# Optimization experiments

Measured on AMD Instinct MI355X. Metric: run time of the kernel, lower is better.

Reference implementation:

```python
import jax, jax.numpy as jnp
import numpy as np

WINDOW_SIZE = 11
SIGMA = 1.5
C1 = (0.01 * 1.0) ** 2
C2 = (0.03 * 1.0) ** 2


def _gauss1d(k, sigma):
    x = np.arange(k, dtype=np.float64) - k // 2
    g = np.exp(-(x ** 2) / (2.0 * sigma ** 2)) / (np.sqrt(2.0 * np.pi) * sigma)
    return (g / g.sum()).astype(np.float32)


def _blur3d(x, g):
    # Separable 3D Gaussian blur, SAME padding. Math-equal to the full 11^3
    # kernel conv in the torch code since the 3D window is an outer product
    # of the normalized 1D Gaussian (symmetric, so conv == cross-corr).
    k = g.shape[0]
    p = k // 2
    dn = ('NCDHW', 'OIDHW', 'NCDHW')
    for axis in range(3):
        shape = [1, 1, 1, 1, 1]
        shape[2 + axis] = k
        w = jnp.asarray(g).reshape(shape)
        pad = [(0, 0), (0, 0), (0, 0)]
        pad[axis] = (p, p)
        x = jax.lax.conv_general_dilated(x, w, (1, 1, 1), pad, dimension_numbers=dn)
    return x


def setup_inputs() -> dict:
    key = jax.random.key(0)
    k1, k2 = jax.random.split(key)
    shape = (4, 1, 192, 192, 192)
    gt = jax.random.uniform(k1, shape, dtype=jnp.float32)
    pred = jax.random.uniform(k2, shape, dtype=jnp.float32)
    return {"gt": gt, "pred": pred}


def reference(gt, pred):
    g = _gauss1d(WINDOW_SIZE, SIGMA)
    mux = _blur3d(gt, g)
    muy = _blur3d(pred, g)
    mux_sq = mux * mux
    muy_sq = muy * muy
    mux_muy = mux * muy
    sigmax_sq = _blur3d(gt * gt, g) - mux_sq
    sigmay_sq = _blur3d(pred * pred, g) - muy_sq
    sigmaxy = _blur3d(gt * pred, g) - mux_muy
    ssim_map = ((2.0 * mux_muy + C1) * (2.0 * sigmaxy + C2)) / (
        (mux_sq + muy_sq + C1) * (sigmax_sq + sigmay_sq + C2))
    return jnp.mean(1.0 - ssim_map)
```

## Files before the change

### kernel.cpp

```cpp
#include <hip/hip_runtime.h>
#include <hip/hip_fp16.h>
#include <math.h>

namespace {
constexpr int S = 192;
constexpr long long S2 = (long long)S * S;
constexpr long long S3 = (long long)S * S2;
constexpr int NB = 4;
constexpr int K = 11;
constexpr int R = 5;
constexpr int HCH = 48;
constexpr int DCH = 48;
constexpr float C1f = 1e-4f;
constexpr float C2f = 9e-4f;

struct GaussW { float g[K]; };

__global__ void k_init(double* acc) { *acc = 0.0; }

__global__ void k_final(const double* __restrict__ acc, float* __restrict__ out) {
  out[0] = (float)(acc[0] / (double)(NB * S3));
}


template <int N, bool GUARD>
__device__ __forceinline__ void loadA(const float* pg, const float* pp, int r0,
                                      int w, float (&la)[K], float (&lb)[K]) {
#pragma unroll
  for (int j = 0; j < N; ++j) {
    int r = r0 + j;
    bool ok = !GUARD || ((unsigned)r < (unsigned)S);
    la[j] = ok ? pg[(long long)r * S + w] : 0.f;
    lb[j] = ok ? pp[(long long)r * S + w] : 0.f;
  }
}

template <int N>
__device__ __forceinline__ void commitA(float2 (*rb)[208], int w,
                                        const float (&la)[K], const float (&lb)[K]) {
#pragma unroll
  for (int j = 0; j < N; ++j) rb[j][8 + w] = make_float2(la[j], lb[j]);
}

template <int NROWS, bool EMITALL>
__device__ __forceinline__ void consumeA(
    const float2 (*rb)[208], int w, const GaussW& Wt,
    float2 (&w01)[K], float2 (&w23)[K], float (&w4v)[K],
    __half2* p01, __half2* p23, __half* p4, long long obase, int hbase) {
#pragma unroll
  for (int j = 0; j < NROWS; ++j) {
    float2 s01 = make_float2(0.f, 0.f), s23 = make_float2(0.f, 0.f);
    float s4 = 0.f;
#pragma unroll
    for (int i = 0; i < K; ++i) {
      float2 ab = rb[j][w + 3 + i];
      float g = Wt.g[i];
      s01.x = fmaf(g, ab.x, s01.x);
      s01.y = fmaf(g, ab.y, s01.y);
      float ta = g * ab.x, tb = g * ab.y;
      s23.x = fmaf(ta, ab.x, s23.x);
      s23.y = fmaf(tb, ab.y, s23.y);
      s4 = fmaf(ta, ab.y, s4);
    }
    w01[j] = s01; w23[j] = s23; w4v[j] = s4;
    if (EMITALL || j == K - 1) {
      float2 m01 = make_float2(0.f, 0.f), m23 = make_float2(0.f, 0.f);
      float m4 = 0.f;
#pragma unroll
      for (int i = 0; i < K; ++i) {
        const int sl = (j + 1 + i) % K;
        float g = Wt.g[i];
        m01.x = fmaf(g, w01[sl].x, m01.x);
        m01.y = fmaf(g, w01[sl].y, m01.y);
        m23.x = fmaf(g, w23[sl].x, m23.x);
        m23.y = fmaf(g, w23[sl].y, m23.y);
        m4 = fmaf(g, w4v[sl], m4);
      }
      long long o = obase + (long long)(hbase + j) * S;
      p01[o] = __floats2half2_rn(m01.x, m01.y);
      p23[o] = __floats2half2_rn(m23.x, m23.y);
      p4[o] = __float2half(m4);
    }
  }
}

__global__ __launch_bounds__(192) void k_blurWH(
    const float* __restrict__ gt, const float* __restrict__ pr,
    __half2* __restrict__ p01, __half2* __restrict__ p23, __half* __restrict__ p4,
    long long in_base, GaussW Wt) {
  __shared__ float2 rowbuf[2][K][208];
  const int w = threadIdx.x;
  const int dz = blockIdx.x;
  const int h0 = (int)blockIdx.y * HCH;
  const long long n = blockIdx.z;
  const float* pg = gt + in_base + (n * S + dz) * S2;
  const float* pp = pr + in_base + (n * S + dz) * S2;
  const long long obase = (n * S + dz) * S2 + w;

  if (w < 176) {
    int j = w >> 4, q = w & 15;
    int idx = (q < 8) ? q : (192 + q);
    rowbuf[0][j][idx] = make_float2(0.f, 0.f);
    rowbuf[1][j][idx] = make_float2(0.f, 0.f);
  }

  float2 w01[K], w23[K];
  float w4v[K];
  float la[K], lb[K];

  loadA<K, true>(pg, pp, h0 - R, w, la, lb);
  commitA<K>(rowbuf[0], w, la, lb);
  __syncthreads();
  loadA<K, false>(pg, pp, h0 + 6, w, la, lb);
  consumeA<K, false>(rowbuf[0], w, Wt, w01, w23, w4v, p01, p23, p4, obase, h0 - 10);
  commitA<K>(rowbuf[1], w, la, lb);
  __syncthreads();
  loadA<K, false>(pg, pp, h0 + 17, w, la, lb);
  consumeA<K, true>(rowbuf[1], w, Wt, w01, w23, w4v, p01, p23, p4, obase, h0 + 1);
  commitA<K>(rowbuf[0], w, la, lb);
  __syncthreads();
  loadA<K, false>(pg, pp, h0 + 28, w, la, lb);
  consumeA<K, true>(rowbuf[0], w, Wt, w01, w23, w4v, p01, p23, p4, obase, h0 + 12);
  commitA<K>(rowbuf[1], w, la, lb);
  __syncthreads();
  loadA<K, true>(pg, pp, h0 + 39, w, la, lb);
  consumeA<K, true>(rowbuf[1], w, Wt, w01, w23, w4v, p01, p23, p4, obase, h0 + 23);
  commitA<K>(rowbuf[0], w, la, lb);
  __syncthreads();
  loadA<3, true>(pg, pp, h0 + 50, w, la, lb);
  consumeA<K, true>(rowbuf[0], w, Wt, w01, w23, w4v, p01, p23, p4, obase, h0 + 34);
  commitA<3>(rowbuf[1], w, la, lb);
  __syncthreads();
  consumeA<3, true>(rowbuf[1], w, Wt, w01, w23, w4v, p01, p23, p4, obase, h0 + 45);
}


template <int N, bool GUARD>
__device__ __forceinline__ void stageB(const __half2* q01, const __half2* q23,
                                       const __half* q4, int plane0,
                                       __half2 (&sa)[K], __half2 (&sb)[K],
                                       __half (&se)[K]) {
  const __half2 z2 = __floats2half2_rn(0.f, 0.f);
  const __half z1 = __float2half(0.f);
#pragma unroll
  for (int j = 0; j < N; ++j) {
    int d = plane0 + j;
    bool ok = !GUARD || ((unsigned)d < (unsigned)S);
    long long o = (long long)d * S2;
    sa[j] = ok ? q01[o] : z2;
    sb[j] = ok ? q23[o] : z2;
    se[j] = ok ? q4[o] : z1;
  }
}

template <int NOUT>
__device__ __forceinline__ void consumeB(
    const __half2 (&sa)[K], const __half2 (&sb)[K], const __half (&se)[K],
    const GaussW& Wt, float2 (&r01)[K], float2 (&r23)[K], float (&r4)[K],
    double& lsum) {
  float fsum = 0.f;
#pragma unroll
  for (int j = 0; j < NOUT; ++j) {
    const int sw = (10 + j) % K;
    r01[sw] = __half22float2(sa[j]);
    r23[sw] = __half22float2(sb[j]);
    r4[sw] = __half2float(se[j]);
    float2 m01 = make_float2(0.f, 0.f), m23 = make_float2(0.f, 0.f);
    float m4 = 0.f;
#pragma unroll
    for (int i = 0; i < K; ++i) {
      const int sl = (j + i) % K;
      float g = Wt.g[i];
      m01.x = fmaf(g, r01[sl].x, m01.x);
      m01.y = fmaf(g, r01[sl].y, m01.y);
      m23.x = fmaf(g, r23[sl].x, m23.x);
      m23.y = fmaf(g, r23[sl].y, m23.y);
      m4 = fmaf(g, r4[sl], m4);
    }
    float mux = m01.x, muy = m01.y, bxx = m23.x, byy = m23.y, bxy = m4;
    float mux2 = mux * mux, muy2 = muy * muy, muxy = mux * muy;
    float sx = bxx - mux2, sy = byy - muy2, sxy = bxy - muxy;
    float num = fmaf(2.f, muxy, C1f) * fmaf(2.f, sxy, C2f);
    float den = (mux2 + muy2 + C1f) * (sx + sy + C2f);
    fsum += 1.f - num * __builtin_amdgcn_rcpf(den);
  }
  lsum += (double)fsum;
}

__global__ __launch_bounds__(192) void k_blurD_ssim(
    const __half2* __restrict__ p01, const __half2* __restrict__ p23,
    const __half* __restrict__ p4, double* __restrict__ acc, GaussW Wt) {
  const int w = threadIdx.x;
  const int h = blockIdx.x;
  const long long n = blockIdx.y;
  const int d0 = (int)blockIdx.z * DCH;
  const long long base = n * S3 + (long long)h * S + w;
  const __half2* q01 = p01 + base;
  const __half2* q23 = p23 + base;
  const __half* q4 = p4 + base;

  float2 r01[K], r23[K];
  float r4[K];
#pragma unroll
  for (int c = 0; c < K - 1; ++c) {
    int d = d0 - R + c;
    if ((unsigned)d < (unsigned)S) {
      long long o = (long long)d * S2;
      r01[c] = __half22float2(q01[o]);
      r23[c] = __half22float2(q23[o]);
      r4[c] = __half2float(q4[o]);
    } else {
      r01[c] = make_float2(0.f, 0.f);
      r23[c] = make_float2(0.f, 0.f);
      r4[c] = 0.f;
    }
  }
  r01[K - 1] = make_float2(0.f, 0.f);
  r23[K - 1] = make_float2(0.f, 0.f);
  r4[K - 1] = 0.f;

  __half2 sa0[K], sb0[K], sa1[K], sb1[K];
  __half se0[K], se1[K];
  double lsum = 0.0;

  stageB<K, false>(q01, q23, q4, d0 + 5, sa0, sb0, se0);
  stageB<K, false>(q01, q23, q4, d0 + 16, sa1, sb1, se1);
  consumeB<K>(sa0, sb0, se0, Wt, r01, r23, r4, lsum);
  stageB<K, false>(q01, q23, q4, d0 + 27, sa0, sb0, se0);
  consumeB<K>(sa1, sb1, se1, Wt, r01, r23, r4, lsum);
  stageB<K, true>(q01, q23, q4, d0 + 38, sa1, sb1, se1);
  consumeB<K>(sa0, sb0, se0, Wt, r01, r23, r4, lsum);
  stageB<4, true>(q01, q23, q4, d0 + 49, sa0, sb0, se0);
  consumeB<K>(sa1, sb1, se1, Wt, r01, r23, r4, lsum);
  consumeB<4>(sa0, sb0, se0, Wt, r01, r23, r4, lsum);

  double v = lsum;
#pragma unroll
  for (int o = 32; o > 0; o >>= 1) v += __shfl_down(v, o, 64);
  __shared__ double wsum[3];
  int lane = threadIdx.x & 63, wv = threadIdx.x >> 6;
  if (lane == 0) wsum[wv] = v;
  __syncthreads();
  if (threadIdx.x == 0) atomicAdd(acc, wsum[0] + wsum[1] + wsum[2]);
}

}

extern "C" void kernel_launch(void* const* d_in, const int* in_sizes, int n_in,
                              void* d_out, int out_size, void* d_ws, size_t ws_size,
                              hipStream_t stream) {
  (void)in_sizes; (void)n_in; (void)out_size;
  const float* gt = (const float*)d_in[0];
  const float* pr = (const float*)d_in[1];
  float* out = (float*)d_out;
  double* acc = (double*)d_ws;

  GaussW W;
  {
    double gg[K], sum = 0.0;
    for (int i = 0; i < K; ++i) {
      double x = (double)(i - K / 2);
      gg[i] = exp(-(x * x) / (2.0 * 1.5 * 1.5)) / (sqrt(2.0 * M_PI) * 1.5);
      sum += gg[i];
    }
    for (int i = 0; i < K; ++i) W.g[i] = (float)(gg[i] / sum);
  }

  auto run = [&](long long base_n, int nb) {
    size_t vox = (size_t)nb * S3;
    __half2* p01 = (__half2*)((char*)d_ws + 256);
    __half2* p23 = p01 + vox;
    __half* p4 = (__half*)(p23 + vox);
    k_blurWH<<<dim3(S, S / HCH, nb), dim3(192), 0, stream>>>(
        gt, pr, p01, p23, p4, base_n * S3, W);
    k_blurD_ssim<<<dim3(S, nb, S / DCH), dim3(192), 0, stream>>>(
        p01, p23, p4, acc, W);
  };
  auto need = [](int nb) { return (size_t)256 + (size_t)nb * S3 * 10; };

  k_init<<<dim3(1), dim3(1), 0, stream>>>(acc);
  if (ws_size >= need(4)) {
    run(0, 4);
  } else if (ws_size >= need(2)) {
    run(0, 2);
    run(2, 2);
  } else {
    for (int g = 0; g < NB; ++g) run(g, 1);
  }
  k_final<<<dim3(1), dim3(1), 0, stream>>>(acc, out);
}
```

Baseline: 455.1 us.

## Interleave half2 intermediates into uint2, single-buffer rows, shrink H chunk

The two separate half2 intermediate planes (means and second moments) are merged into one interleaved uint2 array, so each voxel is written and read with a single 8-byte access instead of two 4-byte ones. The WH blur kernel drops its double-buffered row staging in favour of one shared buffer with load, sync, consume, sync phases, and the H chunk shrinks from 48 to 32 rows, giving more blocks. The intent is fewer memory transactions, lower LDS use and higher occupancy. In exchange, loads no longer overlap compute within a block, and the extra blocks recompute more halo rows.

```diff
diff --git a/kernel.cpp b/kernel.cpp
--- a/kernel.cpp
+++ b/kernel.cpp
@@ -9,7 +9,7 @@
 constexpr int NB = 4;
 constexpr int K = 11;
 constexpr int R = 5;
-constexpr int HCH = 48;
+constexpr int HCH = 32;
 constexpr int DCH = 48;
 constexpr float C1f = 1e-4f;
 constexpr float C2f = 9e-4f;
@@ -23,30 +23,26 @@
 }
 
 
-template <int N, bool GUARD>
-__device__ __forceinline__ void loadA(const float* pg, const float* pp, int r0,
-                                      int w, float (&la)[K], float (&lb)[K]) {
-#pragma unroll
-  for (int j = 0; j < N; ++j) {
+template <int NROWS, bool GUARD>
+__device__ __forceinline__ void stageA(const float* pg, const float* pp, int r0,
+                                       int w, float2 (*rb)[208]) {
+  float la[NROWS], lb[NROWS];
+#pragma unroll
+  for (int j = 0; j < NROWS; ++j) {
     int r = r0 + j;
     bool ok = !GUARD || ((unsigned)r < (unsigned)S);
     la[j] = ok ? pg[(long long)r * S + w] : 0.f;
     lb[j] = ok ? pp[(long long)r * S + w] : 0.f;
   }
-}
-
-template <int N>
-__device__ __forceinline__ void commitA(float2 (*rb)[208], int w,
-                                        const float (&la)[K], const float (&lb)[K]) {
-#pragma unroll
-  for (int j = 0; j < N; ++j) rb[j][8 + w] = make_float2(la[j], lb[j]);
+#pragma unroll
+  for (int j = 0; j < NROWS; ++j) rb[j][8 + w] = make_float2(la[j], lb[j]);
 }
 
 template <int NROWS, bool EMITALL>
 __device__ __forceinline__ void consumeA(
     const float2 (*rb)[208], int w, const GaussW& Wt,
     float2 (&w01)[K], float2 (&w23)[K], float (&w4v)[K],
-    __half2* p01, __half2* p23, __half* p4, long long obase, int hbase) {
+    uint2* p0123, __half* p4, long long obase, int hbase) {
 #pragma unroll
   for (int j = 0; j < NROWS; ++j) {
     float2 s01 = make_float2(0.f, 0.f), s23 = make_float2(0.f, 0.f);
@@ -77,8 +73,12 @@
         m4 = fmaf(g, w4v[sl], m4);
       }
       long long o = obase + (long long)(hbase + j) * S;
-      p01[o] = __floats2half2_rn(m01.x, m01.y);
-      p23[o] = __floats2half2_rn(m23.x, m23.y);
+      __half2 h01 = __floats2half2_rn(m01.x, m01.y);
+      __half2 h23 = __floats2half2_rn(m23.x, m23.y);
+      uint2 v;
+      v.x = __builtin_bit_cast(unsigned, h01);
+      v.y = __builtin_bit_cast(unsigned, h23);
+      p0123[o] = v;
       p4[o] = __float2half(m4);
     }
   }
@@ -86,9 +86,9 @@
 
 __global__ __launch_bounds__(192) void k_blurWH(
     const float* __restrict__ gt, const float* __restrict__ pr,
-    __half2* __restrict__ p01, __half2* __restrict__ p23, __half* __restrict__ p4,
+    uint2* __restrict__ p0123, __half* __restrict__ p4,
     long long in_base, GaussW Wt) {
-  __shared__ float2 rowbuf[2][K][208];
+  __shared__ float2 rowbuf[K][208];
   const int w = threadIdx.x;
   const int dz = blockIdx.x;
   const int h0 = (int)blockIdx.y * HCH;
@@ -99,71 +99,54 @@
 
   if (w < 176) {
     int j = w >> 4, q = w & 15;
-    int idx = (q < 8) ? q : (192 + q);
-    rowbuf[0][j][idx] = make_float2(0.f, 0.f);
-    rowbuf[1][j][idx] = make_float2(0.f, 0.f);
+    rowbuf[j][(q < 8) ? q : (192 + q)] = make_float2(0.f, 0.f);
   }
 
   float2 w01[K], w23[K];
   float w4v[K];
-  float la[K], lb[K];
-
-  loadA<K, true>(pg, pp, h0 - R, w, la, lb);
-  commitA<K>(rowbuf[0], w, la, lb);
-  __syncthreads();
-  loadA<K, false>(pg, pp, h0 + 6, w, la, lb);
-  consumeA<K, false>(rowbuf[0], w, Wt, w01, w23, w4v, p01, p23, p4, obase, h0 - 10);
-  commitA<K>(rowbuf[1], w, la, lb);
-  __syncthreads();
-  loadA<K, false>(pg, pp, h0 + 17, w, la, lb);
-  consumeA<K, true>(rowbuf[1], w, Wt, w01, w23, w4v, p01, p23, p4, obase, h0 + 1);
-  commitA<K>(rowbuf[0], w, la, lb);
-  __syncthreads();
-  loadA<K, false>(pg, pp, h0 + 28, w, la, lb);
-  consumeA<K, true>(rowbuf[0], w, Wt, w01, w23, w4v, p01, p23, p4, obase, h0 + 12);
-  commitA<K>(rowbuf[1], w, la, lb);
-  __syncthreads();
-  loadA<K, true>(pg, pp, h0 + 39, w, la, lb);
-  consumeA<K, true>(rowbuf[1], w, Wt, w01, w23, w4v, p01, p23, p4, obase, h0 + 23);
-  commitA<K>(rowbuf[0], w, la, lb);
-  __syncthreads();
-  loadA<3, true>(pg, pp, h0 + 50, w, la, lb);
-  consumeA<K, true>(rowbuf[0], w, Wt, w01, w23, w4v, p01, p23, p4, obase, h0 + 34);
-  commitA<3>(rowbuf[1], w, la, lb);
-  __syncthreads();
-  consumeA<3, true>(rowbuf[1], w, Wt, w01, w23, w4v, p01, p23, p4, obase, h0 + 45);
+
+  stageA<K, true>(pg, pp, h0 - R, w, rowbuf);
+  __syncthreads();
+  consumeA<K, false>(rowbuf, w, Wt, w01, w23, w4v, p0123, p4, obase, h0 - 10);
+  __syncthreads();
+  stageA<K, false>(pg, pp, h0 + 6, w, rowbuf);
+  __syncthreads();
+  consumeA<K, true>(rowbuf, w, Wt, w01, w23, w4v, p0123, p4, obase, h0 + 1);
+  __syncthreads();
+  stageA<K, false>(pg, pp, h0 + 17, w, rowbuf);
+  __syncthreads();
+  consumeA<K, true>(rowbuf, w, Wt, w01, w23, w4v, p0123, p4, obase, h0 + 12);
+  __syncthreads();
+  stageA<9, true>(pg, pp, h0 + 28, w, rowbuf);
+  __syncthreads();
+  consumeA<9, true>(rowbuf, w, Wt, w01, w23, w4v, p0123, p4, obase, h0 + 23);
 }
 
 
 template <int N, bool GUARD>
-__device__ __forceinline__ void stageB(const __half2* q01, const __half2* q23,
-                                       const __half* q4, int plane0,
-                                       __half2 (&sa)[K], __half2 (&sb)[K],
-                                       __half (&se)[K]) {
-  const __half2 z2 = __floats2half2_rn(0.f, 0.f);
-  const __half z1 = __float2half(0.f);
+__device__ __forceinline__ void stageB(const uint2* q0123, const __half* q4,
+                                       int plane0, uint2 (&sab)[K], __half (&se)[K]) {
 #pragma unroll
   for (int j = 0; j < N; ++j) {
     int d = plane0 + j;
     bool ok = !GUARD || ((unsigned)d < (unsigned)S);
     long long o = (long long)d * S2;
-    sa[j] = ok ? q01[o] : z2;
-    sb[j] = ok ? q23[o] : z2;
-    se[j] = ok ? q4[o] : z1;
+    sab[j] = ok ? q0123[o] : make_uint2(0u, 0u);
+    se[j] = ok ? q4[o] : __float2half(0.f);
   }
 }
 
 template <int NOUT>
 __device__ __forceinline__ void consumeB(
-    const __half2 (&sa)[K], const __half2 (&sb)[K], const __half (&se)[K],
+    const uint2 (&sab)[K], const __half (&se)[K],
     const GaussW& Wt, float2 (&r01)[K], float2 (&r23)[K], float (&r4)[K],
     double& lsum) {
   float fsum = 0.f;
 #pragma unroll
   for (int j = 0; j < NOUT; ++j) {
     const int sw = (10 + j) % K;
-    r01[sw] = __half22float2(sa[j]);
-    r23[sw] = __half22float2(sb[j]);
+    r01[sw] = __half22float2(__builtin_bit_cast(__half2, sab[j].x));
+    r23[sw] = __half22float2(__builtin_bit_cast(__half2, sab[j].y));
     r4[sw] = __half2float(se[j]);
     float2 m01 = make_float2(0.f, 0.f), m23 = make_float2(0.f, 0.f);
     float m4 = 0.f;
@@ -188,15 +171,14 @@
 }
 
 __global__ __launch_bounds__(192) void k_blurD_ssim(
-    const __half2* __restrict__ p01, const __half2* __restrict__ p23,
-    const __half* __restrict__ p4, double* __restrict__ acc, GaussW Wt) {
+    const uint2* __restrict__ p0123, const __half* __restrict__ p4,
+    double* __restrict__ acc, GaussW Wt) {
   const int w = threadIdx.x;
   const int h = blockIdx.x;
   const long long n = blockIdx.y;
   const int d0 = (int)blockIdx.z * DCH;
   const long long base = n * S3 + (long long)h * S + w;
-  const __half2* q01 = p01 + base;
-  const __half2* q23 = p23 + base;
+  const uint2* q0123 = p0123 + base;
   const __half* q4 = p4 + base;
 
   float2 r01[K], r23[K];
@@ -206,8 +188,9 @@
     int d = d0 - R + c;
     if ((unsigned)d < (unsigned)S) {
       long long o = (long long)d * S2;
-      r01[c] = __half22float2(q01[o]);
-      r23[c] = __half22float2(q23[o]);
+      uint2 v = q0123[o];
+      r01[c] = __half22float2(__builtin_bit_cast(__half2, v.x));
+      r23[c] = __half22float2(__builtin_bit_cast(__half2, v.y));
       r4[c] = __half2float(q4[o]);
     } else {
       r01[c] = make_float2(0.f, 0.f);
@@ -219,20 +202,20 @@
   r23[K - 1] = make_float2(0.f, 0.f);
   r4[K - 1] = 0.f;
 
-  __half2 sa0[K], sb0[K], sa1[K], sb1[K];
+  uint2 sab0[K], sab1[K];
   __half se0[K], se1[K];
   double lsum = 0.0;
 
-  stageB<K, false>(q01, q23, q4, d0 + 5, sa0, sb0, se0);
-  stageB<K, false>(q01, q23, q4, d0 + 16, sa1, sb1, se1);
-  consumeB<K>(sa0, sb0, se0, Wt, r01, r23, r4, lsum);
-  stageB<K, false>(q01, q23, q4, d0 + 27, sa0, sb0, se0);
-  consumeB<K>(sa1, sb1, se1, Wt, r01, r23, r4, lsum);
-  stageB<K, true>(q01, q23, q4, d0 + 38, sa1, sb1, se1);
-  consumeB<K>(sa0, sb0, se0, Wt, r01, r23, r4, lsum);
-  stageB<4, true>(q01, q23, q4, d0 + 49, sa0, sb0, se0);
-  consumeB<K>(sa1, sb1, se1, Wt, r01, r23, r4, lsum);
-  consumeB<4>(sa0, sb0, se0, Wt, r01, r23, r4, lsum);
+  stageB<K, false>(q0123, q4, d0 + 5, sab0, se0);
+  stageB<K, false>(q0123, q4, d0 + 16, sab1, se1);
+  consumeB<K>(sab0, se0, Wt, r01, r23, r4, lsum);
+  stageB<K, false>(q0123, q4, d0 + 27, sab0, se0);
+  consumeB<K>(sab1, se1, Wt, r01, r23, r4, lsum);
+  stageB<K, true>(q0123, q4, d0 + 38, sab1, se1);
+  consumeB<K>(sab0, se0, Wt, r01, r23, r4, lsum);
+  stageB<4, true>(q0123, q4, d0 + 49, sab0, se0);
+  consumeB<K>(sab1, se1, Wt, r01, r23, r4, lsum);
+  consumeB<4>(sab0, se0, Wt, r01, r23, r4, lsum);
 
   double v = lsum;
 #pragma unroll
@@ -268,13 +251,12 @@
 
   auto run = [&](long long base_n, int nb) {
     size_t vox = (size_t)nb * S3;
-    __half2* p01 = (__half2*)((char*)d_ws + 256);
-    __half2* p23 = p01 + vox;
-    __half* p4 = (__half*)(p23 + vox);
+    uint2* p0123 = (uint2*)((char*)d_ws + 256);
+    __half* p4 = (__half*)(p0123 + vox);
     k_blurWH<<<dim3(S, S / HCH, nb), dim3(192), 0, stream>>>(
-        gt, pr, p01, p23, p4, base_n * S3, W);
+        gt, pr, p0123, p4, base_n * S3, W);
     k_blurD_ssim<<<dim3(S, nb, S / DCH), dim3(192), 0, stream>>>(
-        p01, p23, p4, acc, W);
+        p0123, p4, acc, W);
   };
   auto need = [](int nb) { return (size_t)256 + (size_t)nb * S3 * 10; };
 
```

Measured after the change: 429.2 us. 5.7% less time.
